# Kernel optimization log

Measured on AMD Instinct MI355X. Metric: run time of the kernel, lower is better.

The kernel has to match this reference:

```python
import jax, jax.numpy as jnp
import numpy as np

BN_EPS = 1e-5


def setup_inputs() -> dict:
    key = jax.random.key(0)
    ks = jax.random.split(key, 9)
    B, C, H, W = 2, 64, 128, 128
    Ci = 32  # inter_channels
    sc = 0.05
    x = jax.random.normal(ks[0], (B, C, H, W), jnp.float32)
    g_w = jax.random.normal(ks[1], (Ci, C), jnp.float32) * sc
    g_b = jax.random.normal(ks[2], (Ci,), jnp.float32) * sc
    theta_w = jax.random.normal(ks[3], (Ci, C), jnp.float32) * sc
    theta_b = jax.random.normal(ks[4], (Ci,), jnp.float32) * sc
    phi_w = jax.random.normal(ks[5], (Ci, C), jnp.float32) * sc
    phi_b = jax.random.normal(ks[6], (Ci,), jnp.float32) * sc
    w_w = jax.random.normal(ks[7], (C, Ci), jnp.float32) * sc
    w_b = jnp.zeros((C,), jnp.float32)
    # BatchNorm affine params (random so the block is non-trivial; the torch
    # code zero-inits them, which would make the whole block an identity).
    bn_gamma = 1.0 + 0.1 * jax.random.normal(ks[8], (C,), jnp.float32)
    bn_beta = jnp.zeros((C,), jnp.float32)
    return dict(x=x, g_w=g_w, g_b=g_b, theta_w=theta_w, theta_b=theta_b,
                phi_w=phi_w, phi_b=phi_b, w_w=w_w, w_b=w_b,
                bn_gamma=bn_gamma, bn_beta=bn_beta)


def reference(x, g_w, g_b, theta_w, theta_b, phi_w, phi_b, w_w, w_b,
              bn_gamma, bn_beta):
    B, C, H, W = x.shape
    Ci = g_w.shape[0]
    H1, W1 = H // 2, W // 2

    def block(xq):  # embedded-gaussian non-local block on one quadrant group [B,C,h,w]
        b, c, h, w = xq.shape
        n = h * w
        xf = xq.reshape(b, c, n)                                  # [B,C,N]
        th = jnp.einsum('oc,bcn->bno', theta_w, xf) + theta_b     # [B,N,Ci]
        ph = jnp.einsum('oc,bcn->bon', phi_w, xf) + phi_b[:, None]  # [B,Ci,N]
        gx = jnp.einsum('oc,bcn->bno', g_w, xf) + g_b             # [B,N,Ci]
        f = jnp.einsum('bno,bom->bnm', th, ph)                    # [B,N,N] affinity
        a = jax.nn.softmax(f, axis=-1)
        y = jnp.einsum('bnm,bmo->bno', a, gx)                     # [B,N,Ci]
        wy = jnp.einsum('co,bno->bcn', w_w, y) + w_b[:, None]     # [B,C,N]
        wy = wy.reshape(b, c, h, w)
        # BatchNorm2d, training-mode batch stats (per quadrant call in torch)
        mu = wy.mean(axis=(0, 2, 3), keepdims=True)
        var = wy.var(axis=(0, 2, 3), keepdims=True)
        bn = (wy - mu) * jax.lax.rsqrt(var + BN_EPS)
        bn = bn * bn_gamma[None, :, None, None] + bn_beta[None, :, None, None]
        return bn + xq                                            # residual

    # split into 4 quadrants: [B,C,H,W] -> [4,B,C,H1,W1] (quadrant-major)
    xq = x.reshape(B, C, 2, H1, 2, W1).transpose(2, 4, 0, 1, 3, 5)
    xq = xq.reshape(4, B, C, H1, W1)
    zq = jax.vmap(block)(xq)                                      # [4,B,C,H1,W1]
    # reassemble
    z = zq.reshape(2, 2, B, C, H1, W1).transpose(2, 3, 0, 4, 1, 5)
    return z.reshape(B, C, H, W)
```

## Files before the change

### kernel.cpp

```cpp
#include <hip/hip_runtime.h>
#include <stdint.h>

typedef __bf16 bf16x8 __attribute__((ext_vector_type(8)));
typedef short  short4v __attribute__((ext_vector_type(4)));
typedef float  floatx4 __attribute__((ext_vector_type(4)));
typedef uint32_t u32x4 __attribute__((ext_vector_type(4)));

#define DI __device__ __forceinline__

DI uint16_t bf1(float a) {
    union { __bf16 h; uint16_t u; } r; r.h = (__bf16)a; return r.u;
}

__global__ __launch_bounds__(256) void proj_kernel(
    const float* __restrict__ x,
    const float* __restrict__ tw, const float* __restrict__ tb,
    const float* __restrict__ pw, const float* __restrict__ pb,
    const float* __restrict__ gw, const float* __restrict__ gb,
    uint16_t* __restrict__ th, uint16_t* __restrict__ phT,
    uint16_t* __restrict__ vP)
{
    __shared__ uint16_t ldsg[32 * 68];
    int nt = blockIdx.x & 63, blk = blockIdx.x >> 6;
    int tid = threadIdx.x, wid = tid >> 6, lane = tid & 63;
    int quad = lane >> 4, low = lane & 15;

    int b = blk & 1, q = blk >> 1, qh = q >> 1, qw = q & 1;
    int pixA = wid * 16 + low;
    const float* xg = x + (size_t)b * 1048576 +
                      (size_t)(qh * 64 + nt) * 128 + qw * 64 + pixA;

    float a0[8], a1[8];
#pragma unroll
    for (int j = 0; j < 8; ++j) {
        a0[j] = xg[(size_t)(quad * 8 + j) * 16384];
        a1[j] = xg[(size_t)(32 + quad * 8 + j) * 16384];
    }
    bf16x8 A0, A1;
#pragma unroll
    for (int j = 0; j < 8; ++j) {
        A0[j] = (__bf16)a0[j];
        A1[j] = (__bf16)a1[j];
    }

    auto dotile = [&](const float* W, const float* Bv, int o0) -> floatx4 {
        floatx4 acc;
        float bias = Bv[o0 + low];
#pragma unroll
        for (int r = 0; r < 4; ++r) acc[r] = bias;
        const float* wr = W + (o0 + low) * 64 + quad * 8;
        floatx4 w0a = *(const floatx4*)(wr);
        floatx4 w0b = *(const floatx4*)(wr + 4);
        floatx4 w1a = *(const floatx4*)(wr + 32);
        floatx4 w1b = *(const floatx4*)(wr + 36);
        bf16x8 B0, B1;
#pragma unroll
        for (int j = 0; j < 4; ++j) {
            B0[j]     = (__bf16)w0a[j];
            B0[j + 4] = (__bf16)w0b[j];
            B1[j]     = (__bf16)w1a[j];
            B1[j + 4] = (__bf16)w1b[j];
        }
        acc = __builtin_amdgcn_mfma_f32_16x16x32_bf16(A0, B0, acc, 0, 0, 0);
        acc = __builtin_amdgcn_mfma_f32_16x16x32_bf16(A1, B1, acc, 0, 0, 0);
        return acc;
    };

    size_t thbase = ((size_t)blk * 4096 + nt * 64 + wid * 16 + quad * 4) * 32;

    floatx4 t0 = dotile(tw, tb, 0), t1 = dotile(tw, tb, 16);
#pragma unroll
    for (int r = 0; r < 4; ++r) {
        th[thbase + r * 32 + low]      = bf1(t0[r] * 1.44269504088896f);
        th[thbase + r * 32 + 16 + low] = bf1(t1[r] * 1.44269504088896f);
    }
    floatx4 p0 = dotile(pw, pb, 0), p1 = dotile(pw, pb, 16);
#pragma unroll
    for (int r = 0; r < 4; ++r) {
        phT[thbase + r * 32 + low]      = bf1(p0[r]);
        phT[thbase + r * 32 + 16 + low] = bf1(p1[r]);
    }
    floatx4 g0 = dotile(gw, gb, 0), g1 = dotile(gw, gb, 16);
#pragma unroll
    for (int r = 0; r < 4; ++r) {
        ldsg[(low)      * 68 + wid * 16 + quad * 4 + r] = bf1(g0[r]);
        ldsg[(16 + low) * 68 + wid * 16 + quad * 4 + r] = bf1(g1[r]);
    }
    __syncthreads();
    {
        int o = tid >> 3, k = (tid & 7) * 8;
        const uint16_t* src = &ldsg[o * 68 + k];
        uint64_t lo = *(const uint64_t*)(src);
        uint64_t hi = *(const uint64_t*)(src + 4);
        union { uint64_t q[2]; u32x4 v; } out;
        out.q[0] = lo; out.q[1] = hi;
        *(u32x4*)(vP + (size_t)blk * 131072 + nt * 2048 + tid * 8) = out.v;
    }
}

__global__ __launch_bounds__(512, 4) void flash_kernel(
    const uint16_t* __restrict__ th, const uint16_t* __restrict__ phT,
    const uint16_t* __restrict__ vP, const float* __restrict__ w_w,
    const float* __restrict__ w_b, float* __restrict__ wy,
    float2* __restrict__ partials)
{
    __shared__ uint16_t ldsK[4][2][64 * 40];
    __shared__ uint16_t ldsV[4][2][32 * 72];
    __shared__ float sred[2][64][2];
    int blk = blockIdx.x & 7;
    int rg  = blockIdx.x >> 3;
    int tid = threadIdx.x, wid = tid >> 6, lane = tid & 63;
    int sp = wid >> 1, qg = wid & 1;
    int lt = tid & 127;
    int quad = lane >> 4, low = lane & 15;
    int n0 = rg * 64 + qg * 32;

    const uint16_t* thB = th  + (size_t)blk * 131072;
    const uint16_t* kG  = phT + (size_t)blk * 131072;
    const uint16_t* vG  = vP  + (size_t)blk * 131072;

    bf16x8 qfA = *(const bf16x8*)(thB + (n0 + low) * 32 + quad * 8);
    bf16x8 qfB = *(const bf16x8*)(thB + (n0 + 16 + low) * 32 + quad * 8);

    const u32x4* kSrc = (const u32x4*)kG + sp * 4096 + lt;
    const u32x4* vSrc = (const u32x4*)vG + sp * 4096 + lt;
    const int kW0 = ((lt >> 2)) * 40 + (lt & 3) * 8;
    const int kW1 = (32 + (lt >> 2)) * 40 + (lt & 3) * 8;
    const int vW0 = ((lt >> 3)) * 72 + (lt & 7) * 8;
    const int vW1 = (16 + (lt >> 3)) * 72 + (lt & 7) * 8;

    u32x4 kr0 = kSrc[0], kr1 = kSrc[128];
    u32x4 vr0 = vSrc[0], vr1 = vSrc[128];
    *(u32x4*)(&ldsK[sp][0][kW0]) = kr0;  *(u32x4*)(&ldsK[sp][0][kW1]) = kr1;
    *(u32x4*)(&ldsV[sp][0][vW0]) = vr0;  *(u32x4*)(&ldsV[sp][0][vW1]) = vr1;
    __syncthreads();

    floatx4 zero = {0.f, 0.f, 0.f, 0.f};
    floatx4 oaA0 = zero, oaA1 = zero, osA = zero;
    floatx4 oaB0 = zero, oaB1 = zero, osB = zero;
    union { uint32_t u[2]; short4v v; } ones;
    ones.u[0] = 0x3F803F80u; ones.u[1] = 0x3F803F80u;

    for (int t = 0; t < 16; ++t) {
        int buf = t & 1;
        if (t < 15) {
            kr0 = kSrc[(t + 1) * 256];  kr1 = kSrc[(t + 1) * 256 + 128];
            vr0 = vSrc[(t + 1) * 256];  vr1 = vSrc[(t + 1) * 256 + 128];
        }
        const uint16_t* Kb = ldsK[sp][buf];
        const uint16_t* Vb = ldsV[sp][buf];
        bf16x8  kf[4]; short4v va[4], vb[4];
#pragma unroll
        for (int c = 0; c < 4; ++c) {
            kf[c] = *(const bf16x8*)(Kb + (c * 16 + low) * 40 + quad * 8);
            va[c] = *(const short4v*)(Vb + low * 72 + c * 16 + quad * 4);
            vb[c] = *(const short4v*)(Vb + (16 + low) * 72 + c * 16 + quad * 4);
        }
        {
            floatx4 sa[4];
#pragma unroll
            for (int c = 0; c < 4; ++c)
                sa[c] = __builtin_amdgcn_mfma_f32_16x16x32_bf16(kf[c], qfA, zero, 0, 0, 0);
            union { __bf16 h[4]; short4v v; } P[4];
#pragma unroll
            for (int c = 0; c < 4; ++c) {
                P[c].h[0] = (__bf16)__builtin_amdgcn_exp2f(sa[c][0]);
                P[c].h[1] = (__bf16)__builtin_amdgcn_exp2f(sa[c][1]);
                P[c].h[2] = (__bf16)__builtin_amdgcn_exp2f(sa[c][2]);
                P[c].h[3] = (__bf16)__builtin_amdgcn_exp2f(sa[c][3]);
            }
#pragma unroll
            for (int c = 0; c < 4; ++c) {
                oaA0 = __builtin_amdgcn_mfma_f32_16x16x16bf16_1k(va[c], P[c].v, oaA0, 0, 0, 0);
                oaA1 = __builtin_amdgcn_mfma_f32_16x16x16bf16_1k(vb[c], P[c].v, oaA1, 0, 0, 0);
                osA  = __builtin_amdgcn_mfma_f32_16x16x16bf16_1k(ones.v, P[c].v, osA, 0, 0, 0);
            }
        }
        {
            floatx4 sa[4];
#pragma unroll
            for (int c = 0; c < 4; ++c)
                sa[c] = __builtin_amdgcn_mfma_f32_16x16x32_bf16(kf[c], qfB, zero, 0, 0, 0);
            union { __bf16 h[4]; short4v v; } P[4];
#pragma unroll
            for (int c = 0; c < 4; ++c) {
                P[c].h[0] = (__bf16)__builtin_amdgcn_exp2f(sa[c][0]);
                P[c].h[1] = (__bf16)__builtin_amdgcn_exp2f(sa[c][1]);
                P[c].h[2] = (__bf16)__builtin_amdgcn_exp2f(sa[c][2]);
                P[c].h[3] = (__bf16)__builtin_amdgcn_exp2f(sa[c][3]);
            }
#pragma unroll
            for (int c = 0; c < 4; ++c) {
                oaB0 = __builtin_amdgcn_mfma_f32_16x16x16bf16_1k(va[c], P[c].v, oaB0, 0, 0, 0);
                oaB1 = __builtin_amdgcn_mfma_f32_16x16x16bf16_1k(vb[c], P[c].v, oaB1, 0, 0, 0);
                osB  = __builtin_amdgcn_mfma_f32_16x16x16bf16_1k(ones.v, P[c].v, osB, 0, 0, 0);
            }
        }
        if (t < 15) {
            *(u32x4*)(&ldsK[sp][buf ^ 1][kW0]) = kr0;
            *(u32x4*)(&ldsK[sp][buf ^ 1][kW1]) = kr1;
            *(u32x4*)(&ldsV[sp][buf ^ 1][vW0]) = vr0;
            *(u32x4*)(&ldsV[sp][buf ^ 1][vW1]) = vr1;
        }
        __syncthreads();
    }

    {
        float* exW = (float*)(&ldsK[0][0][0]);
        int li = tid * 18;
#pragma unroll
        for (int r = 0; r < 4; ++r) {
            exW[li + r]      = oaA0[r];
            exW[li + 4 + r]  = oaA1[r];
            exW[li + 9 + r]  = oaB0[r];
            exW[li + 13 + r] = oaB1[r];
        }
        exW[li + 8]  = osA[0];
        exW[li + 17] = osB[0];
    }
    __syncthreads();
    floatx4 cA0 = zero, cA1 = zero, cB0 = zero, cB1 = zero;
    float cosA = 0.f, cosB = 0.f;
    {
        const float* exR = (const float*)(&ldsK[0][0][0]);
#pragma unroll
        for (int s = 0; s < 4; ++s) {
            const float* p = exR + (s * 128 + lt) * 18;
#pragma unroll
            for (int r = 0; r < 4; ++r) {
                cA0[r] += p[r];
                cA1[r] += p[4 + r];
                cB0[r] += p[9 + r];
                cB1[r] += p[13 + r];
            }
            cosA += p[8];
            cosB += p[17];
        }
    }

    float rinvA = 1.0f / cosA, rinvB = 1.0f / cosB;
    union { __bf16 h[4]; short4v v; } YA0, YA1, YB0, YB1;
#pragma unroll
    for (int r = 0; r < 4; ++r) {
        YA0.h[r] = (__bf16)(cA0[r] * rinvA);
        YA1.h[r] = (__bf16)(cA1[r] * rinvA);
        YB0.h[r] = (__bf16)(cB0[r] * rinvB);
        YB1.h[r] = (__bf16)(cB1[r] * rinvB);
    }

    float* wyB = wy + (size_t)blk * 262144;
    int nA = n0 + low, nB = n0 + 16 + low;
    int ct = sp;
    {
        floatx4 accA, accB;
#pragma unroll
        for (int r = 0; r < 4; ++r) {
            accA[r] = w_b[ct * 16 + quad * 4 + r];
            accB[r] = accA[r];
        }
        floatx4 w0 = *(const floatx4*)(w_w + (ct * 16 + low) * 32 + quad * 4);
        floatx4 w1 = *(const floatx4*)(w_w + (ct * 16 + low) * 32 + 16 + quad * 4);
        union { __bf16 h[4]; short4v v; } W0, W1;
#pragma unroll
        for (int r = 0; r < 4; ++r) {
            W0.h[r] = (__bf16)w0[r];
            W1.h[r] = (__bf16)w1[r];
        }
        accA = __builtin_amdgcn_mfma_f32_16x16x16bf16_1k(W0.v, YA0.v, accA, 0, 0, 0);
        accA = __builtin_amdgcn_mfma_f32_16x16x16bf16_1k(W1.v, YA1.v, accA, 0, 0, 0);
        accB = __builtin_amdgcn_mfma_f32_16x16x16bf16_1k(W0.v, YB0.v, accB, 0, 0, 0);
        accB = __builtin_amdgcn_mfma_f32_16x16x16bf16_1k(W1.v, YB1.v, accB, 0, 0, 0);
#pragma unroll
        for (int r = 0; r < 4; ++r) {
            int ch = ct * 16 + quad * 4 + r;
            wyB[(size_t)ch * 4096 + nA] = accA[r];
            wyB[(size_t)ch * 4096 + nB] = accB[r];
            float s = accA[r] + accB[r];
            float ss = accA[r] * accA[r] + accB[r] * accB[r];
            s += __shfl_xor(s, 1); ss += __shfl_xor(ss, 1);
            s += __shfl_xor(s, 2); ss += __shfl_xor(ss, 2);
            s += __shfl_xor(s, 4); ss += __shfl_xor(ss, 4);
            s += __shfl_xor(s, 8); ss += __shfl_xor(ss, 8);
            if (low == 0) {
                sred[qg][ch][0] = s;
                sred[qg][ch][1] = ss;
            }
        }
    }
    __syncthreads();
    if (tid < 64) {
        float s  = sred[0][tid][0] + sred[1][tid][0];
        float ss = sred[0][tid][1] + sred[1][tid][1];
        partials[((size_t)blk * 64 + rg) * 64 + tid] = make_float2(s, ss);
    }
}

__global__ __launch_bounds__(64) void stats_kernel(
    const float2* __restrict__ partials, const float* __restrict__ gamma,
    const float* __restrict__ beta, float2* __restrict__ stats)
{
    int q = blockIdx.x >> 6, c = blockIdx.x & 63;
    int t = threadIdx.x;
    float2 p0 = partials[(((size_t)(q * 2 + 0)) * 64 + t) * 64 + c];
    float2 p1 = partials[(((size_t)(q * 2 + 1)) * 64 + t) * 64 + c];
    float S = p0.x + p1.x, SS = p0.y + p1.y;
    S += __shfl_xor(S, 1);  SS += __shfl_xor(SS, 1);
    S += __shfl_xor(S, 2);  SS += __shfl_xor(SS, 2);
    S += __shfl_xor(S, 4);  SS += __shfl_xor(SS, 4);
    S += __shfl_xor(S, 8);  SS += __shfl_xor(SS, 8);
    S += __shfl_xor(S, 16); SS += __shfl_xor(SS, 16);
    S += __shfl_xor(S, 32); SS += __shfl_xor(SS, 32);
    if (t == 0) {
        float mu  = S * (1.0f / 8192.0f);
        float var = SS * (1.0f / 8192.0f) - mu * mu;
        float scale = gamma[c] * rsqrtf(var + 1e-5f);
        float shift = beta[c] - mu * scale;
        stats[q * 64 + c] = make_float2(scale, shift);
    }
}

__global__ __launch_bounds__(256) void final_kernel(
    const float* __restrict__ wy, const float2* __restrict__ stats,
    const float* __restrict__ x, float* __restrict__ out)
{
    size_t base = ((size_t)blockIdx.x * 256 + threadIdx.x) * 4;
    int n   = (int)(base & 4095);
    int c   = (int)((base >> 12) & 63);
    int blk = (int)(base >> 18);
    int b = blk & 1, q = blk >> 1, qh = q >> 1, qw = q & 1;
    int i = n >> 6, j = n & 63;
    float2 sc = stats[q * 64 + c];
    floatx4 wv = *(const floatx4*)(wy + base);
    size_t xa = ((size_t)(b * 64 + c) * 128 + (qh * 64 + i)) * 128 + qw * 64 + j;
    floatx4 xv = *(const floatx4*)(x + xa);
    floatx4 ov;
#pragma unroll
    for (int k = 0; k < 4; ++k) ov[k] = wv[k] * sc.x + sc.y + xv[k];
    *(floatx4*)(out + xa) = ov;
}

extern "C" void kernel_launch(void* const* d_in, const int* in_sizes, int n_in,
                              void* d_out, int out_size, void* d_ws, size_t ws_size,
                              hipStream_t stream)
{
    const float* x       = (const float*)d_in[0];
    const float* g_w     = (const float*)d_in[1];
    const float* g_b     = (const float*)d_in[2];
    const float* theta_w = (const float*)d_in[3];
    const float* theta_b = (const float*)d_in[4];
    const float* phi_w   = (const float*)d_in[5];
    const float* phi_b   = (const float*)d_in[6];
    const float* w_w     = (const float*)d_in[7];
    const float* w_b     = (const float*)d_in[8];
    const float* gamma   = (const float*)d_in[9];
    const float* beta    = (const float*)d_in[10];

    char* ws = (char*)d_ws;
    uint16_t* th       = (uint16_t*)(ws);
    uint16_t* phT      = (uint16_t*)(ws + (2u << 20));
    uint16_t* vP       = (uint16_t*)(ws + (4u << 20));
    float*    wy       = (float*)(ws + (6u << 20));
    float2*   partials = (float2*)(ws + (14u << 20));
    float2*   stats    = (float2*)(ws + (14u << 20) + (1u << 18));

    proj_kernel  <<<512,  256, 0, stream>>>(x, theta_w, theta_b, phi_w, phi_b,
                                            g_w, g_b, th, phT, vP);
    flash_kernel <<<512,  512, 0, stream>>>(th, phT, vP, w_w, w_b, wy, partials);
    stats_kernel <<<256,  64,  0, stream>>>(partials, gamma, beta, stats);
    final_kernel <<<2048, 256, 0, stream>>>(wy, stats, x, (float*)d_out);
}
```

Baseline: 123.7 us.

## Use 16x16x32 bf16 MFMA for PV and output projection, remap block order

Replaces pairs of 16x16x16 bf16 MFMAs in the P·V accumulation, the row-sum computation and the W output projection with single 16x16x32 MFMAs by packing two K-chunks into 8-wide operands. This halves the MFMA instruction count in the attention inner loop. The proj and final kernels also remap blockIdx so consecutive blocks cover different batch/quadrant groups, which changes the memory access interleaving across CUs. Correctness relies on the packed operand layout matching the 16x16x32 lane mapping for both the P and V operands.

After: 123.3 us. Within noise of the previous version (-0.4%).

```diff
diff --git a/kernel.cpp b/kernel.cpp
--- a/kernel.cpp
+++ b/kernel.cpp
@@ -21,7 +21,7 @@
     uint16_t* __restrict__ vP)
 {
     __shared__ uint16_t ldsg[32 * 68];
-    int nt = blockIdx.x & 63, blk = blockIdx.x >> 6;
+    int blk = blockIdx.x & 7, nt = blockIdx.x >> 3;
     int tid = threadIdx.x, wid = tid >> 6, lane = tid & 63;
     int quad = lane >> 4, low = lane & 15;
 
@@ -138,8 +138,9 @@
     floatx4 zero = {0.f, 0.f, 0.f, 0.f};
     floatx4 oaA0 = zero, oaA1 = zero, osA = zero;
     floatx4 oaB0 = zero, oaB1 = zero, osB = zero;
-    union { uint32_t u[2]; short4v v; } ones;
-    ones.u[0] = 0x3F803F80u; ones.u[1] = 0x3F803F80u;
+    union { uint32_t u[4]; bf16x8 v; } ones8;
+    ones8.u[0] = 0x3F803F80u; ones8.u[1] = 0x3F803F80u;
+    ones8.u[2] = 0x3F803F80u; ones8.u[3] = 0x3F803F80u;
 
     for (int t = 0; t < 16; ++t) {
         int buf = t & 1;
@@ -149,31 +150,37 @@
         }
         const uint16_t* Kb = ldsK[sp][buf];
         const uint16_t* Vb = ldsV[sp][buf];
-        bf16x8  kf[4]; short4v va[4], vb[4];
-#pragma unroll
-        for (int c = 0; c < 4; ++c) {
+        bf16x8 kf[4];
+        union { short4v s[2]; bf16x8 v; } vA2[2], vB2[2];
+#pragma unroll
+        for (int c = 0; c < 4; ++c)
             kf[c] = *(const bf16x8*)(Kb + (c * 16 + low) * 40 + quad * 8);
-            va[c] = *(const short4v*)(Vb + low * 72 + c * 16 + quad * 4);
-            vb[c] = *(const short4v*)(Vb + (16 + low) * 72 + c * 16 + quad * 4);
+#pragma unroll
+        for (int c2 = 0; c2 < 2; ++c2) {
+            vA2[c2].s[0] = *(const short4v*)(Vb + low * 72 + (2*c2)     * 16 + quad * 4);
+            vA2[c2].s[1] = *(const short4v*)(Vb + low * 72 + (2*c2 + 1) * 16 + quad * 4);
+            vB2[c2].s[0] = *(const short4v*)(Vb + (16 + low) * 72 + (2*c2)     * 16 + quad * 4);
+            vB2[c2].s[1] = *(const short4v*)(Vb + (16 + low) * 72 + (2*c2 + 1) * 16 + quad * 4);
         }
         {
             floatx4 sa[4];
 #pragma unroll
             for (int c = 0; c < 4; ++c)
                 sa[c] = __builtin_amdgcn_mfma_f32_16x16x32_bf16(kf[c], qfA, zero, 0, 0, 0);
-            union { __bf16 h[4]; short4v v; } P[4];
-#pragma unroll
-            for (int c = 0; c < 4; ++c) {
-                P[c].h[0] = (__bf16)__builtin_amdgcn_exp2f(sa[c][0]);
-                P[c].h[1] = (__bf16)__builtin_amdgcn_exp2f(sa[c][1]);
-                P[c].h[2] = (__bf16)__builtin_amdgcn_exp2f(sa[c][2]);
-                P[c].h[3] = (__bf16)__builtin_amdgcn_exp2f(sa[c][3]);
-            }
-#pragma unroll
-            for (int c = 0; c < 4; ++c) {
-                oaA0 = __builtin_amdgcn_mfma_f32_16x16x16bf16_1k(va[c], P[c].v, oaA0, 0, 0, 0);
-                oaA1 = __builtin_amdgcn_mfma_f32_16x16x16bf16_1k(vb[c], P[c].v, oaA1, 0, 0, 0);
-                osA  = __builtin_amdgcn_mfma_f32_16x16x16bf16_1k(ones.v, P[c].v, osA, 0, 0, 0);
+            union { __bf16 h[8]; bf16x8 v; } P2[2];
+#pragma unroll
+            for (int c2 = 0; c2 < 2; ++c2) {
+#pragma unroll
+                for (int j = 0; j < 4; ++j) {
+                    P2[c2].h[j]     = (__bf16)__builtin_amdgcn_exp2f(sa[2*c2][j]);
+                    P2[c2].h[4 + j] = (__bf16)__builtin_amdgcn_exp2f(sa[2*c2 + 1][j]);
+                }
+            }
+#pragma unroll
+            for (int c2 = 0; c2 < 2; ++c2) {
+                oaA0 = __builtin_amdgcn_mfma_f32_16x16x32_bf16(vA2[c2].v, P2[c2].v, oaA0, 0, 0, 0);
+                oaA1 = __builtin_amdgcn_mfma_f32_16x16x32_bf16(vB2[c2].v, P2[c2].v, oaA1, 0, 0, 0);
+                osA  = __builtin_amdgcn_mfma_f32_16x16x32_bf16(ones8.v,   P2[c2].v, osA,  0, 0, 0);
             }
         }
         {
@@ -181,19 +188,20 @@
 #pragma unroll
             for (int c = 0; c < 4; ++c)
                 sa[c] = __builtin_amdgcn_mfma_f32_16x16x32_bf16(kf[c], qfB, zero, 0, 0, 0);
-            union { __bf16 h[4]; short4v v; } P[4];
-#pragma unroll
-            for (int c = 0; c < 4; ++c) {
-                P[c].h[0] = (__bf16)__builtin_amdgcn_exp2f(sa[c][0]);
-                P[c].h[1] = (__bf16)__builtin_amdgcn_exp2f(sa[c][1]);
-                P[c].h[2] = (__bf16)__builtin_amdgcn_exp2f(sa[c][2]);
-                P[c].h[3] = (__bf16)__builtin_amdgcn_exp2f(sa[c][3]);
-            }
-#pragma unroll
-            for (int c = 0; c < 4; ++c) {
-                oaB0 = __builtin_amdgcn_mfma_f32_16x16x16bf16_1k(va[c], P[c].v, oaB0, 0, 0, 0);
-                oaB1 = __builtin_amdgcn_mfma_f32_16x16x16bf16_1k(vb[c], P[c].v, oaB1, 0, 0, 0);
-                osB  = __builtin_amdgcn_mfma_f32_16x16x16bf16_1k(ones.v, P[c].v, osB, 0, 0, 0);
+            union { __bf16 h[8]; bf16x8 v; } P2[2];
+#pragma unroll
+            for (int c2 = 0; c2 < 2; ++c2) {
+#pragma unroll
+                for (int j = 0; j < 4; ++j) {
+                    P2[c2].h[j]     = (__bf16)__builtin_amdgcn_exp2f(sa[2*c2][j]);
+                    P2[c2].h[4 + j] = (__bf16)__builtin_amdgcn_exp2f(sa[2*c2 + 1][j]);
+                }
+            }
+#pragma unroll
+            for (int c2 = 0; c2 < 2; ++c2) {
+                oaB0 = __builtin_amdgcn_mfma_f32_16x16x32_bf16(vA2[c2].v, P2[c2].v, oaB0, 0, 0, 0);
+                oaB1 = __builtin_amdgcn_mfma_f32_16x16x32_bf16(vB2[c2].v, P2[c2].v, oaB1, 0, 0, 0);
+                osB  = __builtin_amdgcn_mfma_f32_16x16x32_bf16(ones8.v,   P2[c2].v, osB,  0, 0, 0);
             }
         }
         if (t < 15) {
@@ -239,13 +247,13 @@
     }
 
     float rinvA = 1.0f / cosA, rinvB = 1.0f / cosB;
-    union { __bf16 h[4]; short4v v; } YA0, YA1, YB0, YB1;
+    union { __bf16 h[8]; bf16x8 v; } YA8, YB8;
 #pragma unroll
     for (int r = 0; r < 4; ++r) {
-        YA0.h[r] = (__bf16)(cA0[r] * rinvA);
-        YA1.h[r] = (__bf16)(cA1[r] * rinvA);
-        YB0.h[r] = (__bf16)(cB0[r] * rinvB);
-        YB1.h[r] = (__bf16)(cB1[r] * rinvB);
+        YA8.h[r]     = (__bf16)(cA0[r] * rinvA);
+        YA8.h[4 + r] = (__bf16)(cA1[r] * rinvA);
+        YB8.h[r]     = (__bf16)(cB0[r] * rinvB);
+        YB8.h[4 + r] = (__bf16)(cB1[r] * rinvB);
     }
 
     float* wyB = wy + (size_t)blk * 262144;
@@ -260,16 +268,14 @@
         }
         floatx4 w0 = *(const floatx4*)(w_w + (ct * 16 + low) * 32 + quad * 4);
         floatx4 w1 = *(const floatx4*)(w_w + (ct * 16 + low) * 32 + 16 + quad * 4);
-        union { __bf16 h[4]; short4v v; } W0, W1;
+        union { __bf16 h[8]; bf16x8 v; } W8;
 #pragma unroll
         for (int r = 0; r < 4; ++r) {
-            W0.h[r] = (__bf16)w0[r];
-            W1.h[r] = (__bf16)w1[r];
-        }
-        accA = __builtin_amdgcn_mfma_f32_16x16x16bf16_1k(W0.v, YA0.v, accA, 0, 0, 0);
-        accA = __builtin_amdgcn_mfma_f32_16x16x16bf16_1k(W1.v, YA1.v, accA, 0, 0, 0);
-        accB = __builtin_amdgcn_mfma_f32_16x16x16bf16_1k(W0.v, YB0.v, accB, 0, 0, 0);
-        accB = __builtin_amdgcn_mfma_f32_16x16x16bf16_1k(W1.v, YB1.v, accB, 0, 0, 0);
+            W8.h[r]     = (__bf16)w0[r];
+            W8.h[4 + r] = (__bf16)w1[r];
+        }
+        accA = __builtin_amdgcn_mfma_f32_16x16x32_bf16(W8.v, YA8.v, accA, 0, 0, 0);
+        accB = __builtin_amdgcn_mfma_f32_16x16x32_bf16(W8.v, YB8.v, accB, 0, 0, 0);
 #pragma unroll
         for (int r = 0; r < 4; ++r) {
             int ch = ct * 16 + quad * 4 + r;
@@ -323,7 +329,8 @@
     const float* __restrict__ wy, const float2* __restrict__ stats,
     const float* __restrict__ x, float* __restrict__ out)
 {
-    size_t base = ((size_t)blockIdx.x * 256 + threadIdx.x) * 4;
+    int bid = blockIdx.x;
+    size_t base = (((size_t)(bid & 7) * 256 + (bid >> 3)) * 256 + threadIdx.x) * 4;
     int n   = (int)(base & 4095);
     int c   = (int)((base >> 12) & 63);
     int blk = (int)(base >> 18);
```
